# Kernel optimization log

Hardware: AMD Instinct MI355X
Metric: run time of the kernel (lower is better)

Reference implementation:

```python
import jax, jax.numpy as jnp
import numpy as np

N_HEADS = 8
N_LSTM_LAYERS = 32
HID = 25  # LSTM hidden units == decoder seq_len
EPS = 1e-5


def _layernorm(x, g, b):
    m = x.mean(-1, keepdims=True)
    v = x.var(-1, keepdims=True)  # biased, as torch LayerNorm
    return (x - m) / jnp.sqrt(v + EPS) * g + b


def _mha(q_in, k_in, v_in, Wq, bq, Wk, bk, Wv, bv, Wo, bo):
    B, L, D = q_in.shape
    S = k_in.shape[1]
    E = D // N_HEADS
    q = (q_in @ Wq + bq).reshape(B, L, N_HEADS, E)
    k = (k_in @ Wk + bk).reshape(B, S, N_HEADS, E)
    v = (v_in @ Wv + bv).reshape(B, S, N_HEADS, E)
    scores = jnp.einsum('blhe,bshe->bhls', q, k) / jnp.sqrt(jnp.asarray(E, q.dtype))
    attn = jax.nn.softmax(scores, axis=-1)
    out = jnp.einsum('bhls,bshe->blhe', attn, v).reshape(B, L, D)
    return out @ Wo + bo


def _lstm_layer(inp, W_ih, W_hh, b_ih, b_hh):
    # inp: [B, T, F]; PyTorch gate order i, f, g, o
    B = inp.shape[0]
    h0 = jnp.zeros((B, HID), inp.dtype)
    c0 = jnp.zeros((B, HID), inp.dtype)
    bias = b_ih + b_hh

    def step(carry, x_t):
        h, c = carry
        gates = x_t @ W_ih.T + h @ W_hh.T + bias  # [B, 4H]
        i, f, g, o = jnp.split(gates, 4, axis=-1)
        c = jax.nn.sigmoid(f) * c + jax.nn.sigmoid(i) * jnp.tanh(g)
        h = jax.nn.sigmoid(o) * jnp.tanh(c)
        return (h, c), h

    xs = jnp.swapaxes(inp, 0, 1)  # [T, B, F]
    _, hs = jax.lax.scan(step, (h0, c0), xs)
    return jnp.swapaxes(hs, 0, 1)  # [B, T, H]


def _forward(x, cross,
             Wq_s, bq_s, Wk_s, bk_s, Wv_s, bv_s, Wo_s, bo_s,
             Wq_c, bq_c, Wk_c, bk_c, Wv_c, bv_c, Wo_c, bo_c,
             g1, b1, g2, b2, g3, b3,
             W_ih, W_hh, b_ih, b_hh, Wc, bc):
    x = x + _mha(x, x, x, Wq_s, bq_s, Wk_s, bk_s, Wv_s, bv_s, Wo_s, bo_s)
    x = _layernorm(x, g1, b1)
    x = x + _mha(x, cross, cross, Wq_c, bq_c, Wk_c, bk_c, Wv_c, bv_c, Wo_c, bo_c)
    x = _layernorm(x, g2, b2)
    # LSTM runs over the feature axis: [B, L=25, D=512] -> [B, T=512, F=25]
    y = jnp.swapaxes(x, 1, 2)
    for l in range(N_LSTM_LAYERS):
        y = _lstm_layer(y, W_ih[l], W_hh[l], b_ih[l], b_hh[l])
    # pointwise conv over channels (dim 1 of [B, 512, 25])
    final_y = jnp.einsum('oc,bcl->bol', Wc, y) + bc[None, :, None]
    final_y = jnp.swapaxes(final_y, 1, 2)  # [B, 25, 512]
    return _layernorm(x + final_y, g3, b3)


def setup_inputs() -> dict:
    key = jax.random.key(0)
    ks = jax.random.split(key, 24)
    B, L, S, D = 128, 25, 96, 512

    def rn(k, shape, scale=0.02):
        return jax.random.normal(k, shape, jnp.float32) * scale

    inp = {
        'x': jax.random.normal(ks[0], (B, L, D), jnp.float32),
        'cross': jax.random.normal(ks[1], (B, S, D), jnp.float32),
        'Wq_s': rn(ks[2], (D, D)), 'bq_s': jnp.zeros(D),
        'Wk_s': rn(ks[3], (D, D)), 'bk_s': jnp.zeros(D),
        'Wv_s': rn(ks[4], (D, D)), 'bv_s': jnp.zeros(D),
        'Wo_s': rn(ks[5], (D, D)), 'bo_s': jnp.zeros(D),
        'Wq_c': rn(ks[6], (D, D)), 'bq_c': jnp.zeros(D),
        'Wk_c': rn(ks[7], (D, D)), 'bk_c': jnp.zeros(D),
        'Wv_c': rn(ks[8], (D, D)), 'bv_c': jnp.zeros(D),
        'Wo_c': rn(ks[9], (D, D)), 'bo_c': jnp.zeros(D),
        'g1': jnp.ones(D), 'b1': jnp.zeros(D),
        'g2': jnp.ones(D), 'b2': jnp.zeros(D),
        'g3': jnp.ones(D), 'b3': jnp.zeros(D),
        'W_ih': rn(ks[10], (N_LSTM_LAYERS, 4 * HID, HID), 0.1),
        'W_hh': rn(ks[11], (N_LSTM_LAYERS, 4 * HID, HID), 0.1),
        'b_ih': jnp.zeros((N_LSTM_LAYERS, 4 * HID)),
        'b_hh': jnp.zeros((N_LSTM_LAYERS, 4 * HID)),
        'Wc': rn(ks[12], (D, D)), 'bc': jnp.zeros(D),
    }
    return inp


def reference(x, cross,
              Wq_s, bq_s, Wk_s, bk_s, Wv_s, bv_s, Wo_s, bo_s,
              Wq_c, bq_c, Wk_c, bk_c, Wv_c, bv_c, Wo_c, bo_c,
              g1, b1, g2, b2, g3, b3,
              W_ih, W_hh, b_ih, b_hh, Wc, bc):
    return _forward(x, cross,
                    Wq_s, bq_s, Wk_s, bk_s, Wv_s, bv_s, Wo_s, bo_s,
                    Wq_c, bq_c, Wk_c, bk_c, Wv_c, bv_c, Wo_c, bo_c,
                    g1, b1, g2, b2, g3, b3,
                    W_ih, W_hh, b_ih, b_hh, Wc, bc)
```

## Files before the change

### kernel.cpp

```cpp
#include <hip/hip_runtime.h>


#define EPS_LN 1e-5f

typedef _Float16 h2v __attribute__((ext_vector_type(2)));
typedef _Float16 h8v __attribute__((ext_vector_type(8)));
typedef float    f4v __attribute__((ext_vector_type(4)));

#if defined(__has_builtin)
#if __has_builtin(__builtin_amdgcn_fdot2)
#define HAVE_FDOT2 1
#endif
#if __has_builtin(__builtin_amdgcn_rcpf)
#define HAVE_RCPF 1
#endif
#endif

__device__ __forceinline__ float fdot2(h2v a, h2v b, float c) {
#ifdef HAVE_FDOT2
  return __builtin_amdgcn_fdot2(a, b, c, false);
#else
  return c + (float)a.x * (float)b.x + (float)a.y * (float)b.y;
#endif
}
__device__ __forceinline__ h2v bch2(unsigned int u) {
  return __builtin_bit_cast(h2v, u);
}
__device__ __forceinline__ float rcp_fast(float x) {
#ifdef HAVE_RCPF
  return __builtin_amdgcn_rcpf(x);
#else
  return 1.f / x;
#endif
}
__device__ __forceinline__ float sigm_fast(float x) {
  return rcp_fast(1.f + __expf(-x));
}
__device__ __forceinline__ float tanh_fast(float x) {
  return 1.f - 2.f * rcp_fast(1.f + __expf(2.f * x));
}

struct WPtrs { const float* p[9]; };

__global__ __launch_bounds__(256)
void prep_weights(WPtrs w, _Float16* __restrict__ dst) {
  __shared__ float tile[32][33];
  const int z = blockIdx.z;
  const int tx = threadIdx.x & 31, ty = threadIdx.x >> 5;
  const int bx = blockIdx.x, by = blockIdx.y;
  const float* in = w.p[z];
  _Float16* outp = dst + (size_t)z * 262144;
  if (z < 8) {
#pragma unroll
    for (int i = 0; i < 4; i++)
      tile[ty + i * 8][tx] = in[(size_t)(by * 32 + ty + i * 8) * 512 + bx * 32 + tx];
    __syncthreads();
#pragma unroll
    for (int i = 0; i < 4; i++)
      outp[(size_t)(bx * 32 + ty + i * 8) * 512 + by * 32 + tx] = (_Float16)tile[tx][ty + i * 8];
  } else {
#pragma unroll
    for (int i = 0; i < 4; i++) {
      size_t off = (size_t)(by * 32 + ty + i * 8) * 512 + bx * 32 + tx;
      outp[off] = (_Float16)in[off];
    }
  }
}

__global__ __launch_bounds__(256)
void gemm3(const float* __restrict__ A,
           const _Float16* __restrict__ BT0, const _Float16* __restrict__ BT1,
           const _Float16* __restrict__ BT2,
           const float* __restrict__ bias0, const float* __restrict__ bias1,
           const float* __restrict__ bias2,
           float* __restrict__ C0, float* __restrict__ C1, float* __restrict__ C2,
           int M) {
  __shared__ _Float16 Asld[64 * 40];
  __shared__ _Float16 Bsld[64 * 40];
  const int t = threadIdx.x;
  const int which = blockIdx.x >> 3;
  const int n0 = (blockIdx.x & 7) * 64;
  const int m0 = blockIdx.y * 64;
  const _Float16* BT = (which == 0) ? BT0 : (which == 1) ? BT1 : BT2;
  const float* bias  = (which == 0) ? bias0 : (which == 1) ? bias1 : bias2;
  float* C           = (which == 0) ? C0 : (which == 1) ? C1 : C2;

  const int r = t >> 2, q = t & 3;
  const int w = t >> 6;
  const int lane = t & 63;
  const int lm = lane & 15, q8 = lane >> 4;

  f4v acc[4] = {};
  for (int k0 = 0; k0 < 512; k0 += 32) {
    __syncthreads();
    float4 f0 = *(const float4*)&A[(size_t)(m0 + r) * 512 + k0 + q * 8];
    float4 f1 = *(const float4*)&A[(size_t)(m0 + r) * 512 + k0 + q * 8 + 4];
    h8v hvv = {(_Float16)f0.x, (_Float16)f0.y, (_Float16)f0.z, (_Float16)f0.w,
               (_Float16)f1.x, (_Float16)f1.y, (_Float16)f1.z, (_Float16)f1.w};
    *(h8v*)&Asld[r * 40 + q * 8] = hvv;
    *(uint4*)&Bsld[r * 40 + q * 8] = *(const uint4*)&BT[(size_t)(n0 + r) * 512 + k0 + q * 8];
    __syncthreads();
    h8v a = *(const h8v*)&Asld[(w * 16 + lm) * 40 + q8 * 8];
#pragma unroll
    for (int nt = 0; nt < 4; nt++) {
      h8v b = *(const h8v*)&Bsld[(nt * 16 + lm) * 40 + q8 * 8];
      acc[nt] = __builtin_amdgcn_mfma_f32_16x16x32_f16(a, b, acc[nt], 0, 0, 0);
    }
  }
#pragma unroll
  for (int nt = 0; nt < 4; nt++) {
    int gn = n0 + nt * 16 + lm;
    float bv = bias[gn];
#pragma unroll
    for (int rg = 0; rg < 4; rg++) {
      int gm = m0 + w * 16 + q8 * 4 + rg;
      C[(size_t)gm * 512 + gn] = acc[nt][rg] + bv;
    }
  }
}

template <int S>
__global__ __launch_bounds__(256)
void attn_scores(const float* __restrict__ Q, const float* __restrict__ K,
                 float* __restrict__ P) {
  __shared__ float Qs[25][64];
  __shared__ float Ks[S][65];
  const int h = blockIdx.x, b = blockIdx.y, t = threadIdx.x;
  for (int idx = t; idx < 25 * 64; idx += 256) {
    int l = idx >> 6, e = idx & 63;
    Qs[l][e] = Q[(b * 25 + l) * 512 + h * 64 + e];
  }
  for (int idx = t; idx < S * 64; idx += 256) {
    int s = idx >> 6, e = idx & 63;
    Ks[s][e] = K[(b * S + s) * 512 + h * 64 + e];
  }
  __syncthreads();
  float* Pb = P + (size_t)(b * 8 + h) * 25 * S;
  for (int idx = t; idx < 25 * S; idx += 256) {
    int l = idx / S, s = idx % S;
    float acc = 0.f;
#pragma unroll
    for (int e = 0; e < 64; e++) acc += Qs[l][e] * Ks[s][e];
    Pb[idx] = acc * 0.125f;
  }
}

template <int S>
__global__ __launch_bounds__(256)
void attn_out(const float* __restrict__ P, const float* __restrict__ V,
              float* __restrict__ O) {
  __shared__ float Ps[25][S];
  __shared__ float Vs[S][64];
  const int h = blockIdx.x, b = blockIdx.y, t = threadIdx.x;
  const float* Pb = P + (size_t)(b * 8 + h) * 25 * S;
  for (int idx = t; idx < 25 * S; idx += 256) Ps[idx / S][idx % S] = Pb[idx];
  for (int idx = t; idx < S * 64; idx += 256) {
    int s = idx >> 6, e = idx & 63;
    Vs[s][e] = V[(b * S + s) * 512 + h * 64 + e];
  }
  __syncthreads();
  if (t < 25) {
    float mx = -1e30f;
    for (int s = 0; s < S; s++) mx = fmaxf(mx, Ps[t][s]);
    float sum = 0.f;
    for (int s = 0; s < S; s++) { float p = __expf(Ps[t][s] - mx); Ps[t][s] = p; sum += p; }
    float r = 1.f / sum;
    for (int s = 0; s < S; s++) Ps[t][s] *= r;
  }
  __syncthreads();
  for (int idx = t; idx < 25 * 64; idx += 256) {
    int l = idx >> 6, e = idx & 63;
    float acc = 0.f;
    for (int s = 0; s < S; s++) acc += Ps[l][s] * Vs[s][e];
    O[(b * 25 + l) * 512 + h * 64 + e] = acc;
  }
}

__global__ __launch_bounds__(128)
void add_ln(const float* __restrict__ a, const float* __restrict__ b,
            const float* __restrict__ gw, const float* __restrict__ bw,
            float* __restrict__ out) {
  const int row = blockIdx.x, t = threadIdx.x;
  float4 va = ((const float4*)(a + (size_t)row * 512))[t];
  float4 vb = ((const float4*)(b + (size_t)row * 512))[t];
  float4 v = make_float4(va.x + vb.x, va.y + vb.y, va.z + vb.z, va.w + vb.w);
  float s = v.x + v.y + v.z + v.w;
  float q = v.x * v.x + v.y * v.y + v.z * v.z + v.w * v.w;
#pragma unroll
  for (int off = 32; off > 0; off >>= 1) {
    s += __shfl_down(s, off);
    q += __shfl_down(q, off);
  }
  __shared__ float red[4];
  if ((t & 63) == 0) { red[(t >> 6) * 2] = s; red[(t >> 6) * 2 + 1] = q; }
  __syncthreads();
  float S_ = red[0] + red[2], Q_ = red[1] + red[3];
  float mean = S_ * (1.f / 512.f);
  float var  = Q_ * (1.f / 512.f) - mean * mean;
  float inv  = rsqrtf(var + EPS_LN);
  float4 g4 = ((const float4*)gw)[t];
  float4 b4 = ((const float4*)bw)[t];
  float4 o;
  o.x = (v.x - mean) * inv * g4.x + b4.x;
  o.y = (v.y - mean) * inv * g4.y + b4.y;
  o.z = (v.z - mean) * inv * g4.z + b4.z;
  o.w = (v.w - mean) * inv * g4.w + b4.w;
  ((float4*)(out + (size_t)row * 512))[t] = o;
}

__global__ void transpose_dl(const float* __restrict__ in, float* __restrict__ outp) {
  const int b = blockIdx.x, t = threadIdx.x;
  for (int idx = t; idx < 25 * 512; idx += 256) {
    int l2 = idx / 512, c = idx % 512;
    outp[((size_t)b * 25 + l2) * 512 + c] = in[((size_t)b * 512 + c) * 25 + l2];
  }
}

__global__ __launch_bounds__(256)
void prep_x0r(const float* __restrict__ x2, _Float16* __restrict__ X0) {
  __shared__ float tile[25][516];
  const int b = blockIdx.x, t = threadIdx.x;
  for (int idx = t; idx < 25 * 512; idx += 256) {
    int u = idx >> 9, d = idx & 511;
    tile[u][d] = x2[((size_t)b * 25 + u) * 512 + d];
  }
  __syncthreads();
  for (int idx = t; idx < 512 * 32; idx += 256) {
    int d = idx >> 5, u = idx & 31;
    X0[((size_t)b * 512 + d) * 32 + u] = (u < 25) ? (_Float16)tile[u][d] : (_Float16)0.f;
  }
}

#define NLAY 32
#define NGRP 16
#define BGRP 8
#define CHT  8
#define NCHK 64
#define RSLOTS 64
#define RCHK (RSLOTS / CHT)
#define RLAY ((size_t)128 * RSLOTS * 32)

__device__ __forceinline__ int ld_rlx(int* p) {
  return __hip_atomic_load(p, __ATOMIC_RELAXED, __HIP_MEMORY_SCOPE_AGENT);
}
__device__ __forceinline__ void st_rlx(int* p, int v) {
  __hip_atomic_store(p, v, __ATOMIC_RELAXED, __HIP_MEMORY_SCOPE_AGENT);
}
__device__ __forceinline__ unsigned long long ldq_rlx(const unsigned long long* p) {
  return __hip_atomic_load(p, __ATOMIC_RELAXED, __HIP_MEMORY_SCOPE_AGENT);
}
__device__ __forceinline__ void sth_rlx(_Float16* p, _Float16 v) {
  __hip_atomic_store((unsigned short*)p, __builtin_bit_cast(unsigned short, v),
                     __ATOMIC_RELAXED, __HIP_MEMORY_SCOPE_AGENT);
}

__global__ __launch_bounds__(256) __attribute__((amdgpu_waves_per_eu(2, 2)))
void lstm_pipeline(const _Float16* __restrict__ X0, float* __restrict__ yout,
                   _Float16* __restrict__ ring, int* __restrict__ prod,
                   int* __restrict__ cons,
                   const float* __restrict__ Wih, const float* __restrict__ Whh,
                   const float* __restrict__ bih, const float* __restrict__ bhh) {
  const int l = blockIdx.x / NGRP;
  const int g = blockIdx.x % NGRP;
  const int t = threadIdx.x;
  const int u  = t & 31;
  const int bi = t >> 5;
  const bool active = (u < 25);

  __shared__ _Float16 xbuf[CHT][BGRP][32];
  __shared__ _Float16 hbuf[BGRP][32];

  h2v wih2[4][13], whh2[4][13];
  float bias_r[4];
  float c_reg = 0.f;
  {
    const int uc = active ? u : 24;
#pragma unroll
    for (int j = 0; j < 4; j++) {
      const float* wi = &Wih[((size_t)l * 100 + j * 25 + uc) * 25];
      const float* wh = &Whh[((size_t)l * 100 + j * 25 + uc) * 25];
#pragma unroll
      for (int k = 0; k < 13; k++) {
        float alo = wi[2 * k], ahi = (2 * k + 1 < 25) ? wi[2 * k + 1] : 0.f;
        float blo = wh[2 * k], bhi = (2 * k + 1 < 25) ? wh[2 * k + 1] : 0.f;
        wih2[j][k] = h2v{(_Float16)alo, (_Float16)ahi};
        whh2[j][k] = h2v{(_Float16)blo, (_Float16)bhi};
      }
      bias_r[j] = bih[l * 100 + j * 25 + uc] + bhh[l * 100 + j * 25 + uc];
    }
  }
  for (int idx = t; idx < BGRP * 32; idx += 256) (&hbuf[0][0])[idx] = (_Float16)0.f;
  __syncthreads();

  _Float16* ring_out = ring + (size_t)l * RLAY
                       + ((size_t)(g * BGRP + bi) * RSLOTS) * 32 + u;
  float* yout_out = yout + ((size_t)(g * BGRP + bi) * 512) * 25 + u;

  const int s_tc = t >> 5, s_b2 = (t >> 2) & 7, s_seg = t & 3;

  for (int n = 0; n < NCHK; n++) {
    if (t == 0) {
      if (l > 0) {
        int* p = &prod[(l - 1) * NGRP + g];
        while (ld_rlx(p) < n + 1) __builtin_amdgcn_s_sleep(1);
      }
      if (l < NLAY - 1 && n >= RCHK) {
        int* p = &cons[(l + 1) * NGRP + g];
        while (ld_rlx(p) < n - RCHK + 1) __builtin_amdgcn_s_sleep(1);
      }
    }
    __syncthreads();
    {
      const int tg = n * CHT + s_tc;
      if (l == 0) {
        const uint4* p = (const uint4*)(X0
            + (((size_t)(g * BGRP + s_b2) * 512) + tg) * 32 + s_seg * 8);
        *(uint4*)&xbuf[s_tc][s_b2][s_seg * 8] = *p;
      } else {
        const unsigned long long* p = (const unsigned long long*)(ring
            + (size_t)(l - 1) * RLAY
            + (((size_t)(g * BGRP + s_b2) * RSLOTS) + (tg & (RSLOTS - 1))) * 32
            + s_seg * 8);
        unsigned long long a = ldq_rlx(p);
        unsigned long long b = ldq_rlx(p + 1);
        *(uint4*)&xbuf[s_tc][s_b2][s_seg * 8] =
            make_uint4((unsigned)a, (unsigned)(a >> 32),
                       (unsigned)b, (unsigned)(b >> 32));
      }
    }
    __syncthreads();
    if (t == 0 && l > 0) st_rlx(&cons[l * NGRP + g], n + 1);

    float ax[CHT][4];
    if (active) {
#pragma unroll
      for (int tc = 0; tc < CHT; tc++) {
        const unsigned int* xr = (const unsigned int*)&xbuf[tc][bi][0];
        uint4 xa = *(const uint4*)(xr);
        uint4 xb = *(const uint4*)(xr + 4);
        uint4 xc = *(const uint4*)(xr + 8);
        unsigned int xd = xr[12];
        h2v xk[13] = {bch2(xa.x), bch2(xa.y), bch2(xa.z), bch2(xa.w),
                      bch2(xb.x), bch2(xb.y), bch2(xb.z), bch2(xb.w),
                      bch2(xc.x), bch2(xc.y), bch2(xc.z), bch2(xc.w),
                      bch2(xd)};
        float a0 = bias_r[0], a1 = bias_r[1], a2 = bias_r[2], a3 = bias_r[3];
#pragma unroll
        for (int k = 0; k < 13; k++) {
          a0 = fdot2(wih2[0][k], xk[k], a0);
          a1 = fdot2(wih2[1][k], xk[k], a1);
          a2 = fdot2(wih2[2][k], xk[k], a2);
          a3 = fdot2(wih2[3][k], xk[k], a3);
        }
        ax[tc][0] = a0; ax[tc][1] = a1; ax[tc][2] = a2; ax[tc][3] = a3;
      }
    }

#pragma unroll
    for (int tc = 0; tc < CHT; tc++) {
      const int tg = n * CHT + tc;
      if (active) {
        const unsigned int* hr = (const unsigned int*)&hbuf[bi][0];
        uint4 ha = *(const uint4*)(hr);
        uint4 hb = *(const uint4*)(hr + 4);
        uint4 hc = *(const uint4*)(hr + 8);
        unsigned int hd = hr[12];
        h2v hk[13] = {bch2(ha.x), bch2(ha.y), bch2(ha.z), bch2(ha.w),
                      bch2(hb.x), bch2(hb.y), bch2(hb.z), bch2(hb.w),
                      bch2(hc.x), bch2(hc.y), bch2(hc.z), bch2(hc.w),
                      bch2(hd)};
        float a0 = ax[tc][0], a1 = ax[tc][1], a2 = ax[tc][2], a3 = ax[tc][3];
#pragma unroll
        for (int k = 0; k < 13; k++) {
          a0 = fdot2(whh2[0][k], hk[k], a0);
          a1 = fdot2(whh2[1][k], hk[k], a1);
          a2 = fdot2(whh2[2][k], hk[k], a2);
          a3 = fdot2(whh2[3][k], hk[k], a3);
        }
        float si = sigm_fast(a0);
        float sf = sigm_fast(a1);
        float so = sigm_fast(a3);
        c_reg = sf * c_reg + si * tanh_fast(a2);
        float h = so * tanh_fast(c_reg);
        _Float16 h16 = (_Float16)h;
        hbuf[bi][u] = h16;
        if (l == NLAY - 1)
          yout_out[(size_t)tg * 25] = h;
        else
          sth_rlx(ring_out + (size_t)(tg & (RSLOTS - 1)) * 32, h16);
      }
    }
    asm volatile("s_waitcnt vmcnt(0)" ::: "memory");
    __syncthreads();
    if (t == 0 && l < NLAY - 1) st_rlx(&prod[l * NGRP + g], n + 1);
  }
}

extern "C" void kernel_launch(void* const* d_in, const int* in_sizes, int n_in,
                              void* d_out, int out_size, void* d_ws, size_t ws_size,
                              hipStream_t stream) {
  const float* x     = (const float*)d_in[0];
  const float* cross = (const float*)d_in[1];
  const float* Wq_s = (const float*)d_in[2];  const float* bq_s = (const float*)d_in[3];
  const float* Wk_s = (const float*)d_in[4];  const float* bk_s = (const float*)d_in[5];
  const float* Wv_s = (const float*)d_in[6];  const float* bv_s = (const float*)d_in[7];
  const float* Wo_s = (const float*)d_in[8];  const float* bo_s = (const float*)d_in[9];
  const float* Wq_c = (const float*)d_in[10]; const float* bq_c = (const float*)d_in[11];
  const float* Wk_c = (const float*)d_in[12]; const float* bk_c = (const float*)d_in[13];
  const float* Wv_c = (const float*)d_in[14]; const float* bv_c = (const float*)d_in[15];
  const float* Wo_c = (const float*)d_in[16]; const float* bo_c = (const float*)d_in[17];
  const float* g1 = (const float*)d_in[18]; const float* b1 = (const float*)d_in[19];
  const float* g2 = (const float*)d_in[20]; const float* b2 = (const float*)d_in[21];
  const float* g3 = (const float*)d_in[22]; const float* b3 = (const float*)d_in[23];
  const float* Wih = (const float*)d_in[24];
  const float* Whh = (const float*)d_in[25];
  const float* bih = (const float*)d_in[26];
  const float* bhh = (const float*)d_in[27];
  const float* Wc  = (const float*)d_in[28]; const float* bc = (const float*)d_in[29];
  float* out = (float*)d_out;
  float* ws  = (float*)d_ws;

  constexpr size_t A  = 1638400;
  constexpr size_t C6 = 6291456;
  float* x1    = ws;
  float* Qc    = ws + A;
  float* Qs    = ws + 2 * A;
  float* Ks    = ws + 3 * A;
  float* Vs    = ws + 4 * A;
  float* attns = ws + 5 * A;
  float* tmp   = ws + 6 * A;
  float* Ps    = ws + 7 * A;
  float* Kc    = ws + 2 * A;
  float* Vc    = ws + 2 * A + C6;
  float* attnc = ws + 2 * A + 2 * C6;
  float* Pc    = attnc + A;
  float* tmp2  = ws + 6 * A;
  float* x2    = ws + 3 * A;
  _Float16* X0b  = (_Float16*)(ws + 4 * A);
  float*    youtb = ws + 5 * A;
  _Float16* ringb = (_Float16*)(ws + 6 * A);
  float* ytb   = ws + 2 * A;
  float* fy    = ws + 5 * A;
  _Float16* WTall = (_Float16*)(ws + 20000000);
  int* ctr = (int*)(ws + 21179648);

  dim3 blk(256);
  WPtrs wpq;
  wpq.p[0] = Wq_s; wpq.p[1] = Wk_s; wpq.p[2] = Wv_s; wpq.p[3] = Wo_s;
  wpq.p[4] = Wq_c; wpq.p[5] = Wk_c; wpq.p[6] = Wv_c; wpq.p[7] = Wo_c;
  wpq.p[8] = Wc;
  prep_weights<<<dim3(16, 16, 9), blk, 0, stream>>>(wpq, WTall);
  hipMemsetAsync(ctr, 0, 1024 * sizeof(int), stream);
  _Float16* WT[9];
  for (int i = 0; i < 9; i++) WT[i] = WTall + (size_t)i * 262144;

  gemm3<<<dim3(24, 50), blk, 0, stream>>>(x, WT[0], WT[1], WT[2],
                                          bq_s, bk_s, bv_s, Qs, Ks, Vs, 3200);
  attn_scores<25><<<dim3(8, 128), blk, 0, stream>>>(Qs, Ks, Ps);
  attn_out<25><<<dim3(8, 128), blk, 0, stream>>>(Ps, Vs, attns);
  gemm3<<<dim3(8, 50), blk, 0, stream>>>(attns, WT[3], WT[3], WT[3],
                                         bo_s, bo_s, bo_s, tmp, tmp, tmp, 3200);
  add_ln<<<3200, 128, 0, stream>>>(x, tmp, g1, b1, x1);
  gemm3<<<dim3(8, 50), blk, 0, stream>>>(x1, WT[4], WT[4], WT[4],
                                         bq_c, bq_c, bq_c, Qc, Qc, Qc, 3200);
  gemm3<<<dim3(16, 192), blk, 0, stream>>>(cross, WT[5], WT[6], WT[6],
                                           bk_c, bv_c, bv_c, Kc, Vc, Vc, 12288);
  attn_scores<96><<<dim3(8, 128), blk, 0, stream>>>(Qc, Kc, Pc);
  attn_out<96><<<dim3(8, 128), blk, 0, stream>>>(Pc, Vc, attnc);
  gemm3<<<dim3(8, 50), blk, 0, stream>>>(attnc, WT[7], WT[7], WT[7],
                                         bo_c, bo_c, bo_c, tmp2, tmp2, tmp2, 3200);
  add_ln<<<3200, 128, 0, stream>>>(x1, tmp2, g2, b2, x2);
  prep_x0r<<<128, 256, 0, stream>>>(x2, X0b);
  lstm_pipeline<<<NLAY * NGRP, 256, 0, stream>>>(X0b, youtb, ringb, ctr, ctr + 512,
                                                 Wih, Whh, bih, bhh);
  transpose_dl<<<128, 256, 0, stream>>>(youtb, ytb);
  gemm3<<<dim3(8, 50), blk, 0, stream>>>(ytb, WT[8], WT[8], WT[8],
                                         bc, bc, bc, fy, fy, fy, 3200);
  add_ln<<<3200, 128, 0, stream>>>(x2, fy, g3, b3, out);
}
```

Before: 932.5 us.

## Decouple LSTM pipeline sync to per-wavefront producer/consumer counters

Replaces block-wide __syncthreads and a single thread-0 flag per block with per-wavefront flags, so each of the 4 waves (2 batch rows each) spins, loads its own slice of the ring, and publishes its own progress independently. This removes block barriers from the inner chunk loop of the 32-layer wavefront pipeline, so waves no longer stall on the slowest wave in the block. The counter arrays grow to 64 pipes per layer, and more threads now spin on global atomics, which adds polling traffic.

```diff
diff --git a/kernel.cpp b/kernel.cpp
--- a/kernel.cpp
+++ b/kernel.cpp
@@ -234,6 +234,7 @@
 #define NLAY 32
 #define NGRP 16
 #define BGRP 8
+#define NPIPE 64
 #define CHT  8
 #define NCHK 64
 #define RSLOTS 64
@@ -263,8 +264,11 @@
   const int l = blockIdx.x / NGRP;
   const int g = blockIdx.x % NGRP;
   const int t = threadIdx.x;
+  const int lane = t & 63;
+  const int wv = t >> 6;
   const int u  = t & 31;
   const int bi = t >> 5;
+  const int p  = g * 4 + wv;
   const bool active = (u < 25);
 
   __shared__ _Float16 xbuf[CHT][BGRP][32];
@@ -289,47 +293,50 @@
       bias_r[j] = bih[l * 100 + j * 25 + uc] + bhh[l * 100 + j * 25 + uc];
     }
   }
-  for (int idx = t; idx < BGRP * 32; idx += 256) (&hbuf[0][0])[idx] = (_Float16)0.f;
-  __syncthreads();
+  hbuf[2 * wv + (lane >> 5)][lane & 31] = (_Float16)0.f;
 
   _Float16* ring_out = ring + (size_t)l * RLAY
                        + ((size_t)(g * BGRP + bi) * RSLOTS) * 32 + u;
   float* yout_out = yout + ((size_t)(g * BGRP + bi) * 512) * 25 + u;
 
-  const int s_tc = t >> 5, s_b2 = (t >> 2) & 7, s_seg = t & 3;
+  const int s_tc = lane >> 3;
+  const int s_b2 = 2 * wv + ((lane >> 2) & 1);
+  const int s_seg = lane & 3;
+
+  int* prod_in   = prod + (l - 1) * NPIPE + p;
+  int* prod_out  = prod + l * NPIPE + p;
+  int* cons_self = cons + l * NPIPE + p;
+  int* cons_up   = cons + (l + 1) * NPIPE + p;
 
   for (int n = 0; n < NCHK; n++) {
-    if (t == 0) {
-      if (l > 0) {
-        int* p = &prod[(l - 1) * NGRP + g];
-        while (ld_rlx(p) < n + 1) __builtin_amdgcn_s_sleep(1);
-      }
-      if (l < NLAY - 1 && n >= RCHK) {
-        int* p = &cons[(l + 1) * NGRP + g];
-        while (ld_rlx(p) < n - RCHK + 1) __builtin_amdgcn_s_sleep(1);
-      }
-    }
-    __syncthreads();
+    if (l > 0) {
+      while (ld_rlx(prod_in) < n + 1) __builtin_amdgcn_s_sleep(1);
+    }
+    if (l < NLAY - 1 && n >= RCHK) {
+      while (ld_rlx(cons_up) < n - RCHK + 1) __builtin_amdgcn_s_sleep(1);
+    }
+    asm volatile("" ::: "memory");
+
     {
       const int tg = n * CHT + s_tc;
       if (l == 0) {
-        const uint4* p = (const uint4*)(X0
+        const uint4* p4 = (const uint4*)(X0
             + (((size_t)(g * BGRP + s_b2) * 512) + tg) * 32 + s_seg * 8);
-        *(uint4*)&xbuf[s_tc][s_b2][s_seg * 8] = *p;
+        *(uint4*)&xbuf[s_tc][s_b2][s_seg * 8] = *p4;
       } else {
-        const unsigned long long* p = (const unsigned long long*)(ring
+        const unsigned long long* p8 = (const unsigned long long*)(ring
             + (size_t)(l - 1) * RLAY
             + (((size_t)(g * BGRP + s_b2) * RSLOTS) + (tg & (RSLOTS - 1))) * 32
             + s_seg * 8);
-        unsigned long long a = ldq_rlx(p);
-        unsigned long long b = ldq_rlx(p + 1);
+        unsigned long long a = ldq_rlx(p8);
+        unsigned long long b = ldq_rlx(p8 + 1);
         *(uint4*)&xbuf[s_tc][s_b2][s_seg * 8] =
             make_uint4((unsigned)a, (unsigned)(a >> 32),
                        (unsigned)b, (unsigned)(b >> 32));
       }
     }
-    __syncthreads();
-    if (t == 0 && l > 0) st_rlx(&cons[l * NGRP + g], n + 1);
+    asm volatile("s_waitcnt lgkmcnt(0)" ::: "memory");
+    if (lane == 0 && l > 0) st_rlx(cons_self, n + 1);
 
     float ax[CHT][4];
     if (active) {
@@ -391,8 +398,7 @@
       }
     }
     asm volatile("s_waitcnt vmcnt(0)" ::: "memory");
-    __syncthreads();
-    if (t == 0 && l < NLAY - 1) st_rlx(&prod[l * NGRP + g], n + 1);
+    if (lane == 0 && l < NLAY - 1) st_rlx(prod_out, n + 1);
   }
 }
 
@@ -450,7 +456,7 @@
   wpq.p[4] = Wq_c; wpq.p[5] = Wk_c; wpq.p[6] = Wv_c; wpq.p[7] = Wo_c;
   wpq.p[8] = Wc;
   prep_weights<<<dim3(16, 16, 9), blk, 0, stream>>>(wpq, WTall);
-  hipMemsetAsync(ctr, 0, 1024 * sizeof(int), stream);
+  hipMemsetAsync(ctr, 0, 4096 * sizeof(int), stream);
   _Float16* WT[9];
   for (int i = 0; i < 9; i++) WT[i] = WTall + (size_t)i * 262144;
 
@@ -471,7 +477,7 @@
                                          bo_c, bo_c, bo_c, tmp2, tmp2, tmp2, 3200);
   add_ln<<<3200, 128, 0, stream>>>(x1, tmp2, g2, b2, x2);
   prep_x0r<<<128, 256, 0, stream>>>(x2, X0b);
-  lstm_pipeline<<<NLAY * NGRP, 256, 0, stream>>>(X0b, youtb, ringb, ctr, ctr + 512,
+  lstm_pipeline<<<NLAY * NGRP, 256, 0, stream>>>(X0b, youtb, ringb, ctr, ctr + 2048,
                                                  Wih, Whh, bih, bhh);
   transpose_dl<<<128, 256, 0, stream>>>(youtb, ytb);
   gemm3<<<dim3(8, 50), blk, 0, stream>>>(ytb, WT[8], WT[8], WT[8],
```

After: 912.3 us. 2.2% less time.
